# Performance work log

Hardware: AMD Instinct MI355X
Metric: run time of the kernel (lower is better)

The kernel has to match this reference:

```python
import jax, jax.numpy as jnp
import numpy as np

B, T, D = 2, 2048, 1024
HEADS = 16
MEM = 512
HEAD_DIM = D // HEADS


def setup_inputs() -> dict:
    key = jax.random.key(0)
    k1, k2, k3, k4, k5 = jax.random.split(key, 5)
    x = jax.random.normal(k1, (B, T, D), dtype=jnp.float32)
    w_qkv = jax.random.normal(k2, (3 * D, D), dtype=jnp.float32) * (1.0 / np.sqrt(D))
    w_out = jax.random.normal(k3, (D, D), dtype=jnp.float32) * (1.0 / np.sqrt(D))
    b_out = jax.random.normal(k4, (D,), dtype=jnp.float32) * 0.01
    memory = jax.random.normal(k5, (MEM, D), dtype=jnp.float32)
    return {"x": x, "w_qkv": w_qkv, "w_out": w_out, "b_out": b_out, "memory": memory}


def reference(x, w_qkv, w_out, b_out, memory):
    b, t, d = x.shape
    h, hd = HEADS, HEAD_DIM
    scale = hd ** -0.5
    # QKV projection: [B,T,3D]
    qkv = jnp.einsum('btd,ed->bte', x, w_qkv)
    q, k, v = jnp.split(qkv, 3, axis=-1)
    # [B,H,T,hd]
    q = q.reshape(b, t, h, hd).transpose(0, 2, 1, 3)
    k = k.reshape(b, t, h, hd).transpose(0, 2, 1, 3)
    v = v.reshape(b, t, h, hd).transpose(0, 2, 1, 3)
    # memory K/V: [B,H,MEM,hd] (broadcast over batch)
    mem = memory.reshape(1, MEM, h, hd).transpose(0, 2, 1, 3)
    mem = jnp.broadcast_to(mem, (b, h, MEM, hd))
    k = jnp.concatenate([mem, k], axis=2)
    v = jnp.concatenate([mem, v], axis=2)
    # attention: scores [B,H,T,MEM+T]
    scores = jnp.einsum('bhqd,bhkd->bhqk', q, k) * scale
    weights = jax.nn.softmax(scores, axis=-1)
    out = jnp.einsum('bhqk,bhkd->bhqd', weights, v)
    out = out.transpose(0, 2, 1, 3).reshape(b, t, d)
    return jnp.einsum('btd,ed->bte', out, w_out) + b_out
```

## Files before the change

kernel.cpp:

```cpp
#include <hip/hip_runtime.h>
#include <hip/hip_bf16.h>
#include <stdint.h>

#define B_   2
#define T_   2048
#define D_   1024
#define H_   16
#define HD_  64
#define MEM_ 512
#define KV_  (MEM_ + T_)
#define NIT_ (KV_ / 64)
#define NIT2_ (NIT_ / 2)

using bf16 = __bf16;
typedef __bf16 bf16x8 __attribute__((ext_vector_type(8)));
typedef float  f32x4  __attribute__((ext_vector_type(4)));
typedef short  s16x4  __attribute__((ext_vector_type(4)));
typedef short  s16x8  __attribute__((ext_vector_type(8)));

__device__ __forceinline__ f32x4 mfma16(bf16x8 a, bf16x8 b, f32x4 c) {
  return __builtin_amdgcn_mfma_f32_16x16x32_bf16(a, b, c, 0, 0, 0);
}

__device__ __forceinline__ void gll16(const void* g, void* l) {
  __builtin_amdgcn_global_load_lds(
      (const __attribute__((address_space(1))) unsigned int*)g,
      (__attribute__((address_space(3))) unsigned int*)l, 16, 0, 0);
}

__device__ __forceinline__ unsigned short bf16_bits(float f) {
  bf16 h = (bf16)f;
  return __builtin_bit_cast(unsigned short, h);
}

__device__ __forceinline__ ushort4 pack4(f32x4 v) {
  ushort4 p;
  p.x = bf16_bits(v[0]); p.y = bf16_bits(v[1]);
  p.z = bf16_bits(v[2]); p.w = bf16_bits(v[3]);
  return p;
}

__device__ __forceinline__ bf16x8 cvt8(f32x4 a, f32x4 b) {
  bf16x8 r;
  r[0] = (bf16)a[0]; r[1] = (bf16)a[1]; r[2] = (bf16)a[2]; r[3] = (bf16)a[3];
  r[4] = (bf16)b[0]; r[5] = (bf16)b[1]; r[6] = (bf16)b[2]; r[7] = (bf16)b[3];
  return r;
}

__global__ void prep(const float* __restrict__ x, const float* __restrict__ wq,
                     const float* __restrict__ memory,
                     const float* __restrict__ wout,
                     bf16* __restrict__ xb, bf16* __restrict__ wqb,
                     bf16* __restrict__ mem_k, bf16* __restrict__ mem_vt,
                     bf16* __restrict__ wob) {
  int blk = blockIdx.x;
  if (blk < 3584) {
    const float* s = (blk < 2048) ? x : wq;
    bf16* d = (blk < 2048) ? xb : wqb;
    size_t i = ((size_t)(blk < 2048 ? blk : blk - 2048) * 256 + threadIdx.x) * 8;
    f32x4 a = *(const f32x4*)(s + i);
    f32x4 b = *(const f32x4*)(s + i + 4);
    *(bf16x8*)(d + i) = cvt8(a, b);
  } else if (blk < 3840) {
    int idx8 = ((blk - 3584) * 256 + threadIdx.x) * 8;
    int m = idx8 >> 10, d0 = idx8 & 1023;
    int hh = d0 >> 6, hd0 = d0 & 63;
    f32x4 a = *(const f32x4*)(memory + idx8);
    f32x4 b = *(const f32x4*)(memory + idx8 + 4);
    *(bf16x8*)&mem_k[((size_t)hh * MEM_ + m) * HD_ + hd0] = cvt8(a, b);
  } else if (blk < 4096) {
    int idx = (blk - 3840) * 256 + threadIdx.x;
    int d = idx & 1023;
    int m0 = (idx >> 10) * 8;
    bf16x8 r;
#pragma unroll
    for (int j = 0; j < 8; j++)
      r[j] = (bf16)memory[(size_t)(m0 + j) * D_ + d];
    *(bf16x8*)&mem_vt[(size_t)d * MEM_ + m0] = r;
  } else {
    size_t i = ((size_t)(blk - 4096) * 256 + threadIdx.x) * 8;
    f32x4 a = *(const f32x4*)(wout + i);
    f32x4 b = *(const f32x4*)(wout + i + 4);
    *(bf16x8*)(wob + i) = cvt8(a, b);
  }
}

__global__ void conv_bf16(const float* __restrict__ s, bf16* __restrict__ d) {
  size_t i = ((size_t)blockIdx.x * 256 + threadIdx.x) * 8;
  f32x4 a = *(const f32x4*)(s + i);
  f32x4 b = *(const f32x4*)(s + i + 4);
  *(bf16x8*)(d + i) = cvt8(a, b);
}

template <int EPI, bool APLANE, int NTILE>
__global__ __launch_bounds__(256, 3) void gemm_bt(
    const bf16* __restrict__ A, const bf16* __restrict__ W,
    const float* __restrict__ bias,
    bf16* __restrict__ q_ws, bf16* __restrict__ k_ws, bf16* __restrict__ vt_ws,
    float* __restrict__ Cout, int K) {
  constexpr int NF = NTILE / 32;
  constexpr int NB = NTILE / 32;
  __shared__ __align__(16) bf16 Als[128 * 64];
  __shared__ __align__(16) bf16 Bls[NTILE * 64];
  char* AB = (char*)Als;
  char* BB = (char*)Bls;
  const int nwg = gridDim.x * gridDim.y;
  int lin = blockIdx.y * gridDim.x + blockIdx.x;
  lin = (lin & 7) * (nwg >> 3) + (lin >> 3);
  const int m0 = (lin / gridDim.x) * 128;
  const int n0 = (lin % gridDim.x) * NTILE;
  const int tid = threadIdx.x;
  const int w = tid >> 6;
  const int lane = tid & 63;
  const int lx = lane & 15;
  const int quad = lane >> 4;
  const int amb = (w & 1) * 64;
  const int bnb = (w >> 1) * (NTILE / 2);
  const int srow = tid >> 3;
  const int cs = (tid & 7) ^ (srow & 7);

  f32x4 acc[4][NF];
#pragma unroll
  for (int i = 0; i < 4; i++)
#pragma unroll
    for (int j = 0; j < NF; j++) acc[i][j] = (f32x4){0.f, 0.f, 0.f, 0.f};

  for (int k0 = 0; k0 < K; k0 += 64) {
    const bf16* pa[4];
#pragma unroll
    for (int g = 0; g < 4; g++) {
      int r = srow + 32 * g;
      if constexpr (APLANE) {
        int hh = k0 >> 6, hd = cs * 8;
        int mA = m0 + r;
        pa[g] = A + ((size_t)((mA >> 11) * H_ + hh) * T_ + (mA & 2047)) * HD_ + hd;
      } else {
        pa[g] = A + (size_t)(m0 + r) * K + k0 + cs * 8;
      }
    }
    const bf16* pb[NB];
#pragma unroll
    for (int g = 0; g < NB; g++)
      pb[g] = W + (size_t)(n0 + srow + 32 * g) * K + k0 + cs * 8;

    __syncthreads();
#pragma unroll
    for (int g = 0; g < 4; g++) gll16(pa[g], AB + g * 4096 + tid * 16);
#pragma unroll
    for (int g = 0; g < NB; g++) gll16(pb[g], BB + g * 4096 + tid * 16);
    __syncthreads();

    bf16x8 af[4][2], bfr[NF][2];
    const int rk = (lx & 7) << 4;
#pragma unroll
    for (int mt = 0; mt < 4; mt++)
#pragma unroll
      for (int kh = 0; kh < 2; kh++)
        af[mt][kh] = *(const bf16x8*)(AB + (size_t)(amb + mt * 16 + lx) * 128 +
                                      ((quad * 16 + kh * 64) ^ rk));
#pragma unroll
    for (int nt = 0; nt < NF; nt++)
#pragma unroll
      for (int kh = 0; kh < 2; kh++)
        bfr[nt][kh] = *(const bf16x8*)(BB + (size_t)(bnb + nt * 16 + lx) * 128 +
                                       ((quad * 16 + kh * 64) ^ rk));
#pragma unroll
    for (int kh = 0; kh < 2; kh++)
#pragma unroll
      for (int mt = 0; mt < 4; mt++)
#pragma unroll
        for (int nt = 0; nt < NF; nt++)
          acc[mt][nt] = mfma16(af[mt][kh], bfr[nt][kh], acc[mt][nt]);
  }

  if (EPI == 0) {
#pragma unroll
    for (int mt = 0; mt < 4; mt++) {
      int mbase = m0 + amb + mt * 16 + quad * 4;
      int b = mbase >> 11;
      int t = mbase & 2047;
#pragma unroll
      for (int nt = 0; nt < NF; nt++) {
        int col = n0 + bnb + nt * 16 + lx;
        int which = col >> 10;
        int d = col & 1023;
        int hh = d >> 6, hdi = d & 63;
        int bh = b * H_ + hh;
        if (which == 0) {
#pragma unroll
          for (int r = 0; r < 4; r++)
            q_ws[((size_t)bh * T_ + t + r) * HD_ + hdi] = (bf16)acc[mt][nt][r];
        } else if (which == 1) {
#pragma unroll
          for (int r = 0; r < 4; r++)
            k_ws[((size_t)bh * T_ + t + r) * HD_ + hdi] = (bf16)acc[mt][nt][r];
        } else {
          *(ushort4*)&vt_ws[((size_t)bh * HD_ + hdi) * T_ + t] =
              pack4(acc[mt][nt]);
        }
      }
    }
  } else {
#pragma unroll
    for (int nt = 0; nt < NF; nt++) {
      int col = n0 + bnb + nt * 16 + lx;
      float bias_f = bias[col];
#pragma unroll
      for (int mt = 0; mt < 4; mt++) {
        int mbase = m0 + amb + mt * 16 + quad * 4;
#pragma unroll
        for (int r = 0; r < 4; r++)
          Cout[(size_t)(mbase + r) * D_ + col] = acc[mt][nt][r] + bias_f;
      }
    }
  }
}

__global__ __launch_bounds__(512, 4) void attn_kernel(
    bf16* __restrict__ q_ws, const bf16* __restrict__ k_ws,
    const bf16* __restrict__ vt_ws, const bf16* __restrict__ mem_k,
    const bf16* __restrict__ mem_vt) {
  __shared__ __align__(16) bf16 Kls[2 * 2 * 64 * 64];
  __shared__ __align__(16) bf16 Vls[2 * 2 * 64 * 64];
  char* KB = (char*)Kls;
  char* VB = (char*)Vls;
  const int tid = threadIdx.x;
  const int wh = tid >> 8;
  const int t2 = tid & 255;
  const int w = t2 >> 6;
  const int lane = tid & 63;
  const int lx = lane & 15;
  const int quad = lane >> 4;
  const int bh = blockIdx.x & 31;
  const int qt = blockIdx.x >> 5;
  const int q0 = qt * 128 + w * 32;
  const int h = bh & 15;

  const int srow1 = t2 >> 3;
  const int sc1 = (t2 & 7) ^ (srow1 & 7);

  char* KBh = KB + wh * 16384;
  char* VBh = VB + wh * 16384;

  bf16* qbase = q_ws + ((size_t)bh * T_ + q0) * HD_;

  const bf16* kpl = k_ws + (size_t)bh * T_ * HD_;
  const bf16* vpl = vt_ws + (size_t)bh * HD_ * T_;
  const bf16* mkp = mem_k + (size_t)h * MEM_ * HD_;
  const bf16* mvp = mem_vt + (size_t)h * HD_ * MEM_;

  auto stage = [&](int it2, int bi) {
    const int kv0 = (wh * NIT2_ + it2) * 64;
    const bf16 *kp1, *kp2, *vp1, *vp2;
    if (kv0 < MEM_) {
      kp1 = mkp + (size_t)(kv0 + srow1) * HD_ + sc1 * 8;
      kp2 = kp1 + (size_t)32 * HD_;
      vp1 = mvp + (size_t)srow1 * MEM_ + kv0 + sc1 * 8;
      vp2 = vp1 + (size_t)32 * MEM_;
    } else {
      const int t0 = kv0 - MEM_;
      kp1 = kpl + (size_t)(t0 + srow1) * HD_ + sc1 * 8;
      kp2 = kp1 + (size_t)32 * HD_;
      vp1 = vpl + (size_t)srow1 * T_ + t0 + sc1 * 8;
      vp2 = vp1 + (size_t)32 * T_;
    }
    char* kb = KBh + bi * 8192;
    char* vb = VBh + bi * 8192;
    gll16(kp1, kb + t2 * 16);
    gll16(kp2, kb + t2 * 16 + 4096);
    gll16(vp1, vb + t2 * 16);
    gll16(vp2, vb + t2 * 16 + 4096);
  };

  const float QSCALE = 0.125f * 1.44269504089f;
  bf16x8 qf[2][2];
#pragma unroll
  for (int qg = 0; qg < 2; qg++)
#pragma unroll
    for (int hf = 0; hf < 2; hf++) {
      bf16x8 v = *(const bf16x8*)(qbase + (size_t)(qg * 16 + lx) * HD_ +
                                  hf * 32 + quad * 8);
#pragma unroll
      for (int i = 0; i < 8; i++)
        v[i] = (bf16)((float)v[i] * QSCALE);
      qf[qg][hf] = v;
    }

  bf16x8 ones;
#pragma unroll
  for (int i = 0; i < 8; i++) ones[i] = (bf16)1.0f;

  f32x4 o[4][2];
#pragma unroll
  for (int mt = 0; mt < 4; mt++)
#pragma unroll
    for (int qg = 0; qg < 2; qg++) o[mt][qg] = (f32x4){0.f, 0.f, 0.f, 0.f};
  f32x4 osum[2] = {(f32x4){0.f, 0.f, 0.f, 0.f}, (f32x4){0.f, 0.f, 0.f, 0.f}};

  stage(0, 0);

  for (int it = 0; it < NIT2_; it++) {
    const int cur = it & 1;
    if (it + 1 < NIT2_) {
      stage(it + 1, cur ^ 1);
      asm volatile("s_waitcnt vmcnt(4)" ::: "memory");
    } else {
      asm volatile("s_waitcnt vmcnt(0)" ::: "memory");
    }
    __builtin_amdgcn_s_barrier();
    __builtin_amdgcn_sched_barrier(0);

    const char* KBc = KBh + cur * 8192;
    const char* VBc = VBh + cur * 8192;
    const int sw = (lx & 7) << 4;
    f32x4 s[4][2];
    __builtin_amdgcn_s_setprio(1);
#pragma unroll
    for (int g = 0; g < 4; g++) {
      const char* kb = KBc + (size_t)(g * 16 + lx) * 128;
      bf16x8 ka0 = *(const bf16x8*)(kb + ((quad * 16) ^ sw));
      bf16x8 ka1 = *(const bf16x8*)(kb + ((64 + quad * 16) ^ sw));
#pragma unroll
      for (int qg = 0; qg < 2; qg++) {
        s[g][qg] = (f32x4){0.f, 0.f, 0.f, 0.f};
        s[g][qg] = mfma16(ka0, qf[qg][0], s[g][qg]);
        s[g][qg] = mfma16(ka1, qf[qg][1], s[g][qg]);
      }
    }
    __builtin_amdgcn_s_setprio(0);

    s16x8 pk[2][2];
#pragma unroll
    for (int qg = 0; qg < 2; qg++) {
#pragma unroll
      for (int g = 0; g < 4; g++) {
#pragma unroll
        for (int r = 0; r < 4; r++) {
          float p = __builtin_amdgcn_exp2f(s[g][qg][r]);
          pk[qg][g >> 1][(g & 1) * 4 + r] = (short)bf16_bits(p);
        }
      }
    }

    __builtin_amdgcn_s_setprio(1);
#pragma unroll
    for (int mt = 0; mt < 4; mt++) {
      const char* vb = VBc + (size_t)(mt * 16 + lx) * 128;
#pragma unroll
      for (int p = 0; p < 2; p++) {
        s16x4 lo = *(const s16x4*)(vb + ((p * 64 + quad * 8) ^ sw));
        s16x4 hi = *(const s16x4*)(vb + ((p * 64 + 32 + quad * 8) ^ sw));
        s16x8 cat = __builtin_shufflevector(lo, hi, 0, 1, 2, 3, 4, 5, 6, 7);
        bf16x8 va = __builtin_bit_cast(bf16x8, cat);
#pragma unroll
        for (int qg = 0; qg < 2; qg++)
          o[mt][qg] = mfma16(va, __builtin_bit_cast(bf16x8, pk[qg][p]),
                             o[mt][qg]);
      }
    }
#pragma unroll
    for (int p = 0; p < 2; p++)
#pragma unroll
      for (int qg = 0; qg < 2; qg++)
        osum[qg] = mfma16(ones, __builtin_bit_cast(bf16x8, pk[qg][p]),
                          osum[qg]);
    __builtin_amdgcn_s_setprio(0);

    __builtin_amdgcn_sched_barrier(0);
    __builtin_amdgcn_s_barrier();
  }

  float* OS = (float*)KB;
  float* OSS = (float*)VB;
  if (wh == 1) {
    float* dst = OS + t2 * 32;
#pragma unroll
    for (int mt = 0; mt < 4; mt++)
#pragma unroll
      for (int qg = 0; qg < 2; qg++) {
        int c = mt * 2 + qg;
        *(f32x4*)(dst + ((c ^ (t2 & 7)) * 4)) = o[mt][qg];
      }
    OSS[t2 * 2 + 0] = osum[0][0];
    OSS[t2 * 2 + 1] = osum[1][0];
  }
  __syncthreads();
  if (wh == 0) {
    const float* src = OS + t2 * 32;
    float inv[2] = {1.f / (osum[0][0] + OSS[t2 * 2 + 0]),
                    1.f / (osum[1][0] + OSS[t2 * 2 + 1])};
#pragma unroll
    for (int qg = 0; qg < 2; qg++) {
#pragma unroll
      for (int mt = 0; mt < 4; mt++) {
        int c = mt * 2 + qg;
        f32x4 po = *(const f32x4*)(src + ((c ^ (t2 & 7)) * 4));
        f32x4 ov;
#pragma unroll
        for (int r = 0; r < 4; r++) ov[r] = (o[mt][qg][r] + po[r]) * inv[qg];
        *(ushort4*)(qbase + (size_t)(qg * 16 + lx) * HD_ + mt * 16 + quad * 4)
            = pack4(ov);
      }
    }
  }
}

extern "C" void kernel_launch(void* const* d_in, const int* in_sizes, int n_in,
                              void* d_out, int out_size, void* d_ws,
                              size_t ws_size, hipStream_t stream) {
  const float* x      = (const float*)d_in[0];
  const float* w_qkv  = (const float*)d_in[1];
  const float* w_out  = (const float*)d_in[2];
  const float* b_out  = (const float*)d_in[3];
  const float* memory = (const float*)d_in[4];

  char* ws = (char*)d_ws;
  bf16* q_ws   = (bf16*)(ws);
  bf16* k_ws   = (bf16*)(ws + (8u << 20));
  bf16* vt_ws  = (bf16*)(ws + (16u << 20));
  bf16* mem_k  = (bf16*)(ws + (24u << 20));
  bf16* mem_vt = (bf16*)(ws + (25u << 20));
  float* out = (float*)d_out;

  char* outc = (char*)d_out;
  bf16* xb  = (bf16*)(outc);
  bf16* wqb = (bf16*)(outc + (8u << 20));

  const bool big_ws = ws_size >= (28u << 20);
  bf16* wob = big_ws ? (bf16*)(ws + (26u << 20))
                     : (bf16*)(ws + (8u << 20));

  prep<<<dim3(big_ws ? 4608 : 4096), dim3(256), 0, stream>>>(
      x, w_qkv, memory, w_out, xb, wqb, mem_k, mem_vt, wob);
  gemm_bt<0, false, 128><<<dim3(24, 32), dim3(256), 0, stream>>>(
      xb, wqb, nullptr, q_ws, k_ws, vt_ws, nullptr, 1024);
  attn_kernel<<<dim3(512), dim3(512), 0, stream>>>(
      q_ws, k_ws, vt_ws, mem_k, mem_vt);
  if (!big_ws)
    conv_bf16<<<dim3(512), dim3(256), 0, stream>>>(w_out, wob);
  gemm_bt<1, true, 64><<<dim3(16, 32), dim3(256), 0, stream>>>(
      q_ws, wob, b_out, nullptr, nullptr, nullptr, out, 1024);
}
```

Measured before the change: 179.5 us.

## Software-pipeline attention loop so PV of previous tile overlaps exp of current

Restructures the attention main loop so that each iteration computes QK^T for the current KV tile, then runs the P·V matmul for the previous tile's probabilities, then does exp for the current tile. This lets MFMA work overlap the transcendental exp work. To keep the previous V tile live, the V buffer becomes triple-buffered, which raises LDS use and may reduce occupancy. The loop is also fully unrolled so the modulo-3 buffer indices become constants, at the cost of larger code size.

```diff
diff --git a/kernel.cpp b/kernel.cpp
--- a/kernel.cpp
+++ b/kernel.cpp
@@ -221,7 +221,7 @@
     const bf16* __restrict__ vt_ws, const bf16* __restrict__ mem_k,
     const bf16* __restrict__ mem_vt) {
   __shared__ __align__(16) bf16 Kls[2 * 2 * 64 * 64];
-  __shared__ __align__(16) bf16 Vls[2 * 2 * 64 * 64];
+  __shared__ __align__(16) bf16 Vls[2 * 3 * 64 * 64];
   char* KB = (char*)Kls;
   char* VB = (char*)Vls;
   const int tid = threadIdx.x;
@@ -240,7 +240,7 @@
   const int sc1 = (t2 & 7) ^ (srow1 & 7);
 
   char* KBh = KB + wh * 16384;
-  char* VBh = VB + wh * 16384;
+  char* VBh = VB + wh * 24576;
 
   bf16* qbase = q_ws + ((size_t)bh * T_ + q0) * HD_;
 
@@ -249,7 +249,7 @@
   const bf16* mkp = mem_k + (size_t)h * MEM_ * HD_;
   const bf16* mvp = mem_vt + (size_t)h * HD_ * MEM_;
 
-  auto stage = [&](int it2, int bi) {
+  auto stage = [&](int it2, int kbi, int vbi) {
     const int kv0 = (wh * NIT2_ + it2) * 64;
     const bf16 *kp1, *kp2, *vp1, *vp2;
     if (kv0 < MEM_) {
@@ -264,8 +264,8 @@
       vp1 = vpl + (size_t)srow1 * T_ + t0 + sc1 * 8;
       vp2 = vp1 + (size_t)32 * T_;
     }
-    char* kb = KBh + bi * 8192;
-    char* vb = VBh + bi * 8192;
+    char* kb = KBh + kbi * 8192;
+    char* vb = VBh + vbi * 8192;
     gll16(kp1, kb + t2 * 16);
     gll16(kp2, kb + t2 * 16 + 4096);
     gll16(vp1, vb + t2 * 16);
@@ -297,55 +297,13 @@
     for (int qg = 0; qg < 2; qg++) o[mt][qg] = (f32x4){0.f, 0.f, 0.f, 0.f};
   f32x4 osum[2] = {(f32x4){0.f, 0.f, 0.f, 0.f}, (f32x4){0.f, 0.f, 0.f, 0.f}};
 
-  stage(0, 0);
-
-  for (int it = 0; it < NIT2_; it++) {
-    const int cur = it & 1;
-    if (it + 1 < NIT2_) {
-      stage(it + 1, cur ^ 1);
-      asm volatile("s_waitcnt vmcnt(4)" ::: "memory");
-    } else {
-      asm volatile("s_waitcnt vmcnt(0)" ::: "memory");
-    }
-    __builtin_amdgcn_s_barrier();
-    __builtin_amdgcn_sched_barrier(0);
-
-    const char* KBc = KBh + cur * 8192;
-    const char* VBc = VBh + cur * 8192;
-    const int sw = (lx & 7) << 4;
-    f32x4 s[4][2];
-    __builtin_amdgcn_s_setprio(1);
-#pragma unroll
-    for (int g = 0; g < 4; g++) {
-      const char* kb = KBc + (size_t)(g * 16 + lx) * 128;
-      bf16x8 ka0 = *(const bf16x8*)(kb + ((quad * 16) ^ sw));
-      bf16x8 ka1 = *(const bf16x8*)(kb + ((64 + quad * 16) ^ sw));
-#pragma unroll
-      for (int qg = 0; qg < 2; qg++) {
-        s[g][qg] = (f32x4){0.f, 0.f, 0.f, 0.f};
-        s[g][qg] = mfma16(ka0, qf[qg][0], s[g][qg]);
-        s[g][qg] = mfma16(ka1, qf[qg][1], s[g][qg]);
-      }
-    }
-    __builtin_amdgcn_s_setprio(0);
-
-    s16x8 pk[2][2];
-#pragma unroll
-    for (int qg = 0; qg < 2; qg++) {
-#pragma unroll
-      for (int g = 0; g < 4; g++) {
-#pragma unroll
-        for (int r = 0; r < 4; r++) {
-          float p = __builtin_amdgcn_exp2f(s[g][qg][r]);
-          pk[qg][g >> 1][(g & 1) * 4 + r] = (short)bf16_bits(p);
-        }
-      }
-    }
-
-    __builtin_amdgcn_s_setprio(1);
+  s16x8 pkp[2][2];
+  const int sw = (lx & 7) << 4;
+
+  auto pv_step = [&](const char* VBp) {
 #pragma unroll
     for (int mt = 0; mt < 4; mt++) {
-      const char* vb = VBc + (size_t)(mt * 16 + lx) * 128;
+      const char* vb = VBp + (size_t)(mt * 16 + lx) * 128;
 #pragma unroll
       for (int p = 0; p < 2; p++) {
         s16x4 lo = *(const s16x4*)(vb + ((p * 64 + quad * 8) ^ sw));
@@ -354,7 +312,7 @@
         bf16x8 va = __builtin_bit_cast(bf16x8, cat);
 #pragma unroll
         for (int qg = 0; qg < 2; qg++)
-          o[mt][qg] = mfma16(va, __builtin_bit_cast(bf16x8, pk[qg][p]),
+          o[mt][qg] = mfma16(va, __builtin_bit_cast(bf16x8, pkp[qg][p]),
                              o[mt][qg]);
       }
     }
@@ -362,13 +320,65 @@
     for (int p = 0; p < 2; p++)
 #pragma unroll
       for (int qg = 0; qg < 2; qg++)
-        osum[qg] = mfma16(ones, __builtin_bit_cast(bf16x8, pk[qg][p]),
+        osum[qg] = mfma16(ones, __builtin_bit_cast(bf16x8, pkp[qg][p]),
                           osum[qg]);
+  };
+
+  stage(0, 0, 0);
+
+#pragma unroll
+  for (int it = 0; it < NIT2_; it++) {
+    const int kc = it & 1;
+    const int vprev = (it + 2) % 3;
+    if (it + 1 < NIT2_) {
+      stage(it + 1, kc ^ 1, (it + 1) % 3);
+      asm volatile("s_waitcnt vmcnt(4)" ::: "memory");
+    } else {
+      asm volatile("s_waitcnt vmcnt(0)" ::: "memory");
+    }
+    __builtin_amdgcn_s_barrier();
+    __builtin_amdgcn_sched_barrier(0);
+
+    const char* KBc = KBh + kc * 8192;
+    f32x4 s[4][2];
+    __builtin_amdgcn_s_setprio(1);
+#pragma unroll
+    for (int g = 0; g < 4; g++) {
+      const char* kb = KBc + (size_t)(g * 16 + lx) * 128;
+      bf16x8 ka0 = *(const bf16x8*)(kb + ((quad * 16) ^ sw));
+      bf16x8 ka1 = *(const bf16x8*)(kb + ((64 + quad * 16) ^ sw));
+#pragma unroll
+      for (int qg = 0; qg < 2; qg++) {
+        s[g][qg] = (f32x4){0.f, 0.f, 0.f, 0.f};
+        s[g][qg] = mfma16(ka0, qf[qg][0], s[g][qg]);
+        s[g][qg] = mfma16(ka1, qf[qg][1], s[g][qg]);
+      }
+    }
+    if (it > 0) pv_step(VBh + vprev * 8192);
     __builtin_amdgcn_s_setprio(0);
+
+    s16x8 pkc[2][2];
+#pragma unroll
+    for (int qg = 0; qg < 2; qg++) {
+#pragma unroll
+      for (int g = 0; g < 4; g++) {
+#pragma unroll
+        for (int r = 0; r < 4; r++) {
+          float p = __builtin_amdgcn_exp2f(s[g][qg][r]);
+          pkc[qg][g >> 1][(g & 1) * 4 + r] = (short)bf16_bits(p);
+        }
+      }
+    }
+#pragma unroll
+    for (int a = 0; a < 2; a++)
+#pragma unroll
+      for (int b = 0; b < 2; b++) pkp[a][b] = pkc[a][b];
 
     __builtin_amdgcn_sched_barrier(0);
     __builtin_amdgcn_s_barrier();
   }
+
+  pv_step(VBh + ((NIT2_ - 1) % 3) * 8192);
 
   float* OS = (float*)KB;
   float* OSS = (float*)VB;
```

Result: slower. 266.3 us (+48.4%).
